# Optimization experiments

Measured on AMD Instinct MI355X. Metric: run time of the kernel, lower is better.

The kernel has to match this reference:

```python
import jax, jax.numpy as jnp
import numpy as np

N = 100000
E = 1600000
IN_C = 128
HID = 32
HEADS = 4
OUT_C = 16
NEG_SLOPE = 0.2  # PyG GATConv default


def setup_inputs() -> dict:
    key = jax.random.key(0)
    ks = jax.random.split(key, 10)
    x = jax.random.normal(ks[0], (N, IN_C), dtype=jnp.float32)
    edge_index = jax.random.randint(ks[1], (2, E), 0, N, dtype=jnp.int64)
    # Layer 1 params (heads=4, concat=True)
    s1 = 1.0 / np.sqrt(IN_C)
    W1 = jax.random.normal(ks[2], (IN_C, HEADS * HID), dtype=jnp.float32) * s1
    a_src1 = jax.random.normal(ks[3], (HEADS, HID), dtype=jnp.float32) * s1
    a_dst1 = jax.random.normal(ks[4], (HEADS, HID), dtype=jnp.float32) * s1
    b1 = jnp.zeros((HEADS * HID,), dtype=jnp.float32)
    # Layer 2 params (heads=1, concat=False)
    s2 = 1.0 / np.sqrt(HEADS * HID)
    W2 = jax.random.normal(ks[5], (HEADS * HID, OUT_C), dtype=jnp.float32) * s2
    a_src2 = jax.random.normal(ks[6], (1, OUT_C), dtype=jnp.float32) * s2
    a_dst2 = jax.random.normal(ks[7], (1, OUT_C), dtype=jnp.float32) * s2
    b2 = jnp.zeros((OUT_C,), dtype=jnp.float32)
    return {"x": x, "edge_index": edge_index, "W1": W1, "a_src1": a_src1,
            "a_dst1": a_dst1, "b1": b1, "W2": W2, "a_src2": a_src2,
            "a_dst2": a_dst2, "b2": b2}


def _gat_layer(x, src, dst, W, a_src, a_dst, b, heads, out_c, concat):
    n = x.shape[0]
    h = (x @ W).reshape(n, heads, out_c)            # [N, H, C]
    al_s = jnp.sum(h * a_src, axis=-1)              # [N, H]
    al_d = jnp.sum(h * a_dst, axis=-1)              # [N, H]
    e = al_s[src] + al_d[dst]                       # [E, H]
    e = jnp.where(e > 0, e, NEG_SLOPE * e)          # LeakyReLU(0.2)
    # segment softmax over incoming edges per destination node
    m = jax.ops.segment_max(e, dst, num_segments=n)
    ex = jnp.exp(e - m[dst])
    denom = jax.ops.segment_sum(ex, dst, num_segments=n)
    alpha = ex / denom[dst]                         # [E, H]
    msg = h[src] * alpha[:, :, None]                # [E, H, C]
    out = jax.ops.segment_sum(msg, dst, num_segments=n)  # [N, H, C]
    out = out.reshape(n, heads * out_c) if concat else out.mean(axis=1)
    return out + b


def reference(x, edge_index, W1, a_src1, a_dst1, b1, W2, a_src2, a_dst2, b2):
    n = x.shape[0]
    loops = jnp.arange(n, dtype=edge_index.dtype)
    src = jnp.concatenate([edge_index[0], loops])   # PyG adds self-loops
    dst = jnp.concatenate([edge_index[1], loops])
    h = _gat_layer(x, src, dst, W1, a_src1, a_dst1, b1, HEADS, HID, True)
    h = jax.nn.relu(h)  # dropout is identity at inference
    out = _gat_layer(h, src, dst, W2, a_src2, a_dst2, b2, 1, OUT_C, False)
    return out
```

## Files before the change

### kernel.cpp

```cpp
#include <hip/hip_runtime.h>
#include <hip/hip_fp16.h>

#define N_NODES 100000
#define N_EDGES 1600000
#define E_TOT   (N_EDGES + N_NODES)
#define NEG_SLOPE 0.2f

#define BSH   9
#define BSZ   512
#define NBKT  ((N_NODES + BSZ - 1) / BSZ)
#define CAP   10240
#define EPB   2048
#define PART_B ((E_TOT + EPB - 1) / EPB)
#define GEMM1_B ((N_NODES + 63) / 64)
#define GSTRIDE 16

typedef _Float16 half8_t __attribute__((ext_vector_type(8)));
typedef float f32x4 __attribute__((ext_vector_type(4)));

__device__ __forceinline__ float lrelu(float v) { return v > 0.f ? v : NEG_SLOPE * v; }

__device__ __forceinline__ float f16lo(unsigned u) {
    return __half2float(__ushort_as_half((unsigned short)(u & 0xFFFFu)));
}
__device__ __forceinline__ float f16hi(unsigned u) {
    return __half2float(__ushort_as_half((unsigned short)(u >> 16)));
}

__global__ __launch_bounds__(256) void k_prep(const float* __restrict__ W1,
                                              _Float16* __restrict__ w1t,
                                              int* __restrict__ gcur) {
    int idx = blockIdx.x * 256 + threadIdx.x;
    if (idx < NBKT * GSTRIDE) gcur[idx] = 0;
    int k = idx >> 5;
    int c0 = (idx & 31) * 4;
    float4 wv = ((const float4*)W1)[idx];
    w1t[(c0 + 0) * 128 + k] = (_Float16)wv.x;
    w1t[(c0 + 1) * 128 + k] = (_Float16)wv.y;
    w1t[(c0 + 2) * 128 + k] = (_Float16)wv.z;
    w1t[(c0 + 3) * 128 + k] = (_Float16)wv.w;
}

__global__ __launch_bounds__(256) void k_part_gemm1(
        const int* __restrict__ ei, int* __restrict__ gcur, int* __restrict__ packed,
        const float* __restrict__ x, const _Float16* __restrict__ w1t,
        const float* __restrict__ a_src, const float* __restrict__ a_dst,
        unsigned short* __restrict__ h1h, float* __restrict__ als,
        float* __restrict__ ald) {
    __shared__ __align__(16) union {
        _Float16 cs[64 * 136];
        struct { int lcnt[NBKT]; int gpos[NBKT]; int lcur[NBKT]; } p;
    } sm;
    int t = threadIdx.x;
    if (blockIdx.x < PART_B) {
        int se[8], de[8];
        size_t base = (size_t)blockIdx.x * EPB;
#pragma unroll
        for (int i = 0; i < 8; ++i) {
            size_t e = base + t + i * 256;
            if (e < E_TOT) {
                if (e < N_EDGES) { se[i] = ei[e]; de[i] = ei[N_EDGES + e]; }
                else             { se[i] = (int)(e - N_EDGES); de[i] = se[i]; }
            } else de[i] = -1;
        }
        for (int i = t; i < NBKT; i += 256) sm.p.lcnt[i] = 0;
        __syncthreads();
#pragma unroll
        for (int i = 0; i < 8; ++i)
            if (de[i] >= 0) atomicAdd(&sm.p.lcnt[de[i] >> BSH], 1);
        __syncthreads();
        for (int i = t; i < NBKT; i += 256) {
            int c = sm.p.lcnt[i];
            sm.p.gpos[i] = c ? (i * CAP + atomicAdd(&gcur[i * GSTRIDE], c)) : 0;
            sm.p.lcur[i] = 0;
        }
        __syncthreads();
#pragma unroll
        for (int i = 0; i < 8; ++i) {
            if (de[i] >= 0) {
                int b = de[i] >> BSH;
                int c = atomicAdd(&sm.p.lcur[b], 1);
                packed[sm.p.gpos[b] + c] = ((de[i] & (BSZ - 1)) << 17) | se[i];
            }
        }
        return;
    }
    int nb = (blockIdx.x - PART_B) * 64;
    int wv = t >> 6, lane = t & 63;
    int mn = lane & 15, quad = lane >> 4;
    int an = nb + wv * 16 + mn;
    if (an >= N_NODES) an = 0;
    const float* xrow = x + (size_t)an * 128;
    f32x4 acc[8];
#pragma unroll
    for (int ct = 0; ct < 8; ++ct) acc[ct] = (f32x4){0.f, 0.f, 0.f, 0.f};
#pragma unroll
    for (int kk = 0; kk < 4; ++kk) {
        float4 a0 = *(const float4*)(xrow + kk * 32 + quad * 8);
        float4 a1 = *(const float4*)(xrow + kk * 32 + quad * 8 + 4);
        half8_t af = { (_Float16)a0.x, (_Float16)a0.y, (_Float16)a0.z, (_Float16)a0.w,
                       (_Float16)a1.x, (_Float16)a1.y, (_Float16)a1.z, (_Float16)a1.w };
#pragma unroll
        for (int ct = 0; ct < 8; ++ct) {
            half8_t bf = *(const half8_t*)(w1t + (ct * 16 + mn) * 128 + kk * 32 + quad * 8);
            acc[ct] = __builtin_amdgcn_mfma_f32_16x16x32_f16(af, bf, acc[ct], 0, 0, 0);
        }
    }
#pragma unroll
    for (int ct = 0; ct < 8; ++ct)
#pragma unroll
        for (int r = 0; r < 4; ++r) {
            int nl = wv * 16 + quad * 4 + r;
            sm.cs[nl * 136 + ct * 16 + mn] = (_Float16)acc[ct][r];
        }
    __syncthreads();
    int node = t >> 2, seg = t & 3;
    int gn = nb + node;
    if (gn < N_NODES) {
        const half8_t* hp = (const half8_t*)&sm.cs[node * 136 + seg * 32];
        uint4* gout = (uint4*)(h1h + (size_t)gn * 128 + seg * 32);
        const float4* asp = (const float4*)a_src;
        const float4* adp = (const float4*)a_dst;
        float vs = 0.f, vd = 0.f;
#pragma unroll
        for (int jj = 0; jj < 4; ++jj) {
            half8_t hv = hp[jj];
            gout[jj] = *(const uint4*)&hv;
            float4 aS0 = asp[seg * 8 + jj * 2], aS1 = asp[seg * 8 + jj * 2 + 1];
            float4 aD0 = adp[seg * 8 + jj * 2], aD1 = adp[seg * 8 + jj * 2 + 1];
            vs += (float)hv[0] * aS0.x + (float)hv[1] * aS0.y + (float)hv[2] * aS0.z + (float)hv[3] * aS0.w
                + (float)hv[4] * aS1.x + (float)hv[5] * aS1.y + (float)hv[6] * aS1.z + (float)hv[7] * aS1.w;
            vd += (float)hv[0] * aD0.x + (float)hv[1] * aD0.y + (float)hv[2] * aD0.z + (float)hv[3] * aD0.w
                + (float)hv[4] * aD1.x + (float)hv[5] * aD1.y + (float)hv[6] * aD1.z + (float)hv[7] * aD1.w;
        }
        als[gn * 4 + seg] = vs;
        ald[gn * 4 + seg] = vd;
    }
}

__global__ __launch_bounds__(512) void k_build(const int* __restrict__ packed,
                                               const int* __restrict__ gcur,
                                               int* __restrict__ rowptr,
                                               int* __restrict__ deg,
                                               int* __restrict__ col) {
    int t = threadIdx.x;
    int b = blockIdx.x;
    int nb = b << BSH;
    int ebeg = b * CAP;
    int eend = ebeg + gcur[b * GSTRIDE];
    __shared__ int cnt[BSZ];
    __shared__ int ps[BSZ];
    cnt[t] = 0;
    __syncthreads();
    for (int i = ebeg + t; i < eend; i += 512)
        atomicAdd(&cnt[packed[i] >> 17], 1);
    __syncthreads();
    int v = cnt[t];
    ps[t] = v;
    __syncthreads();
    for (int off = 1; off < 512; off <<= 1) {
        int u = (t >= off) ? ps[t - off] : 0;
        __syncthreads();
        ps[t] += u;
        __syncthreads();
    }
    int myofs = ebeg + ps[t] - v;
    int n = nb + t;
    if (n < N_NODES) { rowptr[n] = myofs; deg[n] = v; }
    __syncthreads();
    cnt[t] = myofs;
    __syncthreads();
    for (int i = ebeg + t; i < eend; i += 512) {
        int p = packed[i];
        int pos = atomicAdd(&cnt[p >> 17], 1);
        col[pos] = p & 0x1FFFF;
    }
}

__global__ __launch_bounds__(256) void k_agg1(const unsigned short* __restrict__ h1h,
                                              const float* __restrict__ als,
                                              const float* __restrict__ ald,
                                              const int* __restrict__ rowptr,
                                              const int* __restrict__ deg,
                                              const int* __restrict__ col,
                                              const float* __restrict__ b1,
                                              float* __restrict__ out1) {
    __shared__ float sex_all[4][64 * 4];
    __shared__ int   scol_all[4][64];
    int w = threadIdx.x >> 6;
    int lane = threadIdx.x & 63;
    int n = blockIdx.x * 4 + w;
    int slot = lane >> 4, cg = lane & 15;
    int hd = cg >> 2;
    float* sex = sex_all[w];
    int* scol = scol_all[w];
    float4 ald4 = ((const float4*)ald)[n];
    int beg = rowptr[n], dtot = deg[n];
    float a0 = 0.f, a1 = 0.f, a2 = 0.f, a3 = 0.f;
    float a4 = 0.f, a5 = 0.f, a6 = 0.f, a7 = 0.f, den = 0.f;
    const float4* als4p = (const float4*)als;
    for (int base = 0; base < dtot; base += 64) {
        int cnt = min(64, dtot - base);
        int myc = 0;
        if (lane < cnt) myc = col[beg + base + lane];
        __asm__ volatile("s_waitcnt lgkmcnt(0)" ::: "memory");
        if (lane < cnt) {
            scol[lane] = myc;
            float4 as4 = als4p[myc];
            float4 e4;
            e4.x = __expf(lrelu(as4.x + ald4.x));
            e4.y = __expf(lrelu(as4.y + ald4.y));
            e4.z = __expf(lrelu(as4.z + ald4.z));
            e4.w = __expf(lrelu(as4.w + ald4.w));
            ((float4*)sex)[lane] = e4;
        }
        __asm__ volatile("s_waitcnt lgkmcnt(0)" ::: "memory");
#pragma unroll 2
        for (int q4 = 0; q4 < cnt; q4 += 4) {
            int myq = q4 + slot;
            int cq = min(myq, cnt - 1);
            int s = scol[cq];
            float ex = (myq < cnt) ? sex[cq * 4 + hd] : 0.f;
            uint4 hv = *(const uint4*)((const char*)h1h + (((size_t)s << 8) + (cg << 4)));
            a0 = fmaf(ex, f16lo(hv.x), a0);
            a1 = fmaf(ex, f16hi(hv.x), a1);
            a2 = fmaf(ex, f16lo(hv.y), a2);
            a3 = fmaf(ex, f16hi(hv.y), a3);
            a4 = fmaf(ex, f16lo(hv.z), a4);
            a5 = fmaf(ex, f16hi(hv.z), a5);
            a6 = fmaf(ex, f16lo(hv.w), a6);
            a7 = fmaf(ex, f16hi(hv.w), a7);
            den += ex;
        }
    }
    a0 += __shfl_xor(a0, 16, 64); a1 += __shfl_xor(a1, 16, 64);
    a2 += __shfl_xor(a2, 16, 64); a3 += __shfl_xor(a3, 16, 64);
    a4 += __shfl_xor(a4, 16, 64); a5 += __shfl_xor(a5, 16, 64);
    a6 += __shfl_xor(a6, 16, 64); a7 += __shfl_xor(a7, 16, 64);
    den += __shfl_xor(den, 16, 64);
    a0 += __shfl_xor(a0, 32, 64); a1 += __shfl_xor(a1, 32, 64);
    a2 += __shfl_xor(a2, 32, 64); a3 += __shfl_xor(a3, 32, 64);
    a4 += __shfl_xor(a4, 32, 64); a5 += __shfl_xor(a5, 32, 64);
    a6 += __shfl_xor(a6, 32, 64); a7 += __shfl_xor(a7, 32, 64);
    den += __shfl_xor(den, 32, 64);
    if (lane < 16) {
        float inv = 1.0f / den;
        float4 bA = ((const float4*)b1)[2 * lane];
        float4 bB = ((const float4*)b1)[2 * lane + 1];
        float4 oA, oB;
        oA.x = fmaxf(fmaf(a0, inv, bA.x), 0.f);
        oA.y = fmaxf(fmaf(a1, inv, bA.y), 0.f);
        oA.z = fmaxf(fmaf(a2, inv, bA.z), 0.f);
        oA.w = fmaxf(fmaf(a3, inv, bA.w), 0.f);
        oB.x = fmaxf(fmaf(a4, inv, bB.x), 0.f);
        oB.y = fmaxf(fmaf(a5, inv, bB.y), 0.f);
        oB.z = fmaxf(fmaf(a6, inv, bB.z), 0.f);
        oB.w = fmaxf(fmaf(a7, inv, bB.w), 0.f);
        ((float4*)out1)[(size_t)n * 32 + 2 * lane]     = oA;
        ((float4*)out1)[(size_t)n * 32 + 2 * lane + 1] = oB;
    }
}

__global__ __launch_bounds__(256) void k_gemm2(const float* __restrict__ out1,
                                               const float* __restrict__ W2,
                                               const float* __restrict__ a_src,
                                               const float* __restrict__ a_dst,
                                               unsigned short* __restrict__ h2h,
                                               float* __restrict__ als,
                                               float* __restrict__ ald) {
    __shared__ float W2s[128 * 16];
    __shared__ float xs[16 * 132];
    int t = threadIdx.x;
#pragma unroll
    for (int i = 0; i < 8; ++i) W2s[t + i * 256] = W2[t + i * 256];
    size_t base = (size_t)blockIdx.x * 16 * 128;
#pragma unroll
    for (int i = 0; i < 8; ++i) {
        int idx = t + i * 256;
        xs[(idx >> 7) * 132 + (idx & 127)] = out1[base + idx];
    }
    __syncthreads();
    int r = t >> 4, c = t & 15;
    float acc = 0.f;
    const float* xr = &xs[r * 132];
#pragma unroll 8
    for (int k = 0; k < 128; ++k) acc = fmaf(xr[k], W2s[k * 16 + c], acc);
    int n = blockIdx.x * 16 + r;
    h2h[(size_t)n * 16 + c] = __half_as_ushort(__float2half(acc));
    float vs = acc * a_src[c];
    float vd = acc * a_dst[c];
#pragma unroll
    for (int off = 8; off >= 1; off >>= 1) {
        vs += __shfl_down(vs, off, 16);
        vd += __shfl_down(vd, off, 16);
    }
    if (c == 0) { als[n] = vs; ald[n] = vd; }
}

__global__ __launch_bounds__(256) void k_agg2(const unsigned short* __restrict__ h2h,
                                              const float* __restrict__ als,
                                              const float* __restrict__ ald,
                                              const int* __restrict__ rowptr,
                                              const int* __restrict__ deg,
                                              const int* __restrict__ col,
                                              const float* __restrict__ b2,
                                              float* __restrict__ out) {
    __shared__ float sex_all[4][64];
    __shared__ int   scol_all[4][64];
    int w = threadIdx.x >> 6;
    int lane = threadIdx.x & 63;
    int n = blockIdx.x * 4 + w;
    int slot = lane >> 2, q = lane & 3;
    float* sex = sex_all[w];
    int* scol = scol_all[w];
    float ad = ald[n];
    int beg = rowptr[n], dtot = deg[n];
    float a0 = 0.f, a1 = 0.f, a2 = 0.f, a3 = 0.f, den = 0.f;
    for (int base = 0; base < dtot; base += 64) {
        int cnt = min(64, dtot - base);
        int myc = 0;
        if (lane < cnt) myc = col[beg + base + lane];
        __asm__ volatile("s_waitcnt lgkmcnt(0)" ::: "memory");
        if (lane < cnt) {
            scol[lane] = myc;
            sex[lane] = __expf(lrelu(als[myc] + ad));
        }
        __asm__ volatile("s_waitcnt lgkmcnt(0)" ::: "memory");
#pragma unroll 2
        for (int q16 = 0; q16 < cnt; q16 += 16) {
            int myq = q16 + slot;
            int cq = min(myq, cnt - 1);
            int s = scol[cq];
            float ex = (myq < cnt) ? sex[cq] : 0.f;
            uint2 hv = *(const uint2*)((const char*)h2h + ((size_t)s * 32u + (q << 3)));
            a0 = fmaf(ex, f16lo(hv.x), a0);
            a1 = fmaf(ex, f16hi(hv.x), a1);
            a2 = fmaf(ex, f16lo(hv.y), a2);
            a3 = fmaf(ex, f16hi(hv.y), a3);
            den += ex;
        }
    }
#pragma unroll
    for (int off = 4; off <= 32; off <<= 1) {
        a0 += __shfl_xor(a0, off, 64);
        a1 += __shfl_xor(a1, off, 64);
        a2 += __shfl_xor(a2, off, 64);
        a3 += __shfl_xor(a3, off, 64);
        den += __shfl_xor(den, off, 64);
    }
    if (slot == 0) {
        float inv = 1.0f / den;
        float4 b4 = ((const float4*)b2)[q];
        float4 o;
        o.x = fmaf(a0, inv, b4.x);
        o.y = fmaf(a1, inv, b4.y);
        o.z = fmaf(a2, inv, b4.z);
        o.w = fmaf(a3, inv, b4.w);
        ((float4*)out)[(size_t)n * 4 + q] = o;
    }
}

extern "C" void kernel_launch(void* const* d_in, const int* in_sizes, int n_in,
                              void* d_out, int out_size, void* d_ws, size_t ws_size,
                              hipStream_t stream) {
    const float* x   = (const float*)d_in[0];
    const int*   ei  = (const int*)d_in[1];
    const float* W1  = (const float*)d_in[2];
    const float* as1 = (const float*)d_in[3];
    const float* ad1 = (const float*)d_in[4];
    const float* b1  = (const float*)d_in[5];
    const float* W2  = (const float*)d_in[6];
    const float* as2 = (const float*)d_in[7];
    const float* ad2 = (const float*)d_in[8];
    const float* b2  = (const float*)d_in[9];
    float* out = (float*)d_out;

    char* ws = (char*)d_ws;
    size_t off = 0;
    auto alloc = [&](size_t bytes) -> void* {
        void* p = ws + off;
        off += (bytes + 255) & ~(size_t)255;
        return p;
    };
    unsigned short* h1h = (unsigned short*)alloc((size_t)N_NODES * 128 * 2);
    float* out1  = (float*)alloc((size_t)N_NODES * 128 * 4);
    float* als1v = (float*)alloc((size_t)N_NODES * 4 * 4);
    float* ald1v = (float*)alloc((size_t)N_NODES * 4 * 4);
    unsigned short* h2h = (unsigned short*)alloc((size_t)N_NODES * 16 * 2);
    float* als2v = (float*)alloc((size_t)N_NODES * 4);
    float* ald2v = (float*)alloc((size_t)N_NODES * 4);
    int* rowptr  = (int*)alloc((size_t)N_NODES * 4);
    int* degv    = (int*)alloc((size_t)N_NODES * 4);
    int* gcur    = (int*)alloc((size_t)NBKT * GSTRIDE * 4);
    _Float16* w1t = (_Float16*)alloc((size_t)128 * 128 * 2);
    int* packed  = (int*)alloc((size_t)NBKT * CAP * 4);
    int* colA    = (int*)alloc((size_t)NBKT * CAP * 4);

    k_prep<<<16, 256, 0, stream>>>(W1, w1t, gcur);
    k_part_gemm1<<<PART_B + GEMM1_B, 256, 0, stream>>>(ei, gcur, packed,
                                                       x, w1t, as1, ad1, h1h, als1v, ald1v);
    k_build<<<NBKT, 512, 0, stream>>>(packed, gcur, rowptr, degv, colA);
    k_agg1<<<N_NODES / 4, 256, 0, stream>>>(h1h, als1v, ald1v, rowptr, degv, colA, b1, out1);
    k_gemm2<<<N_NODES / 16, 256, 0, stream>>>(out1, W2, as2, ad2, h2h, als2v, ald2v);
    k_agg2<<<N_NODES / 4, 256, 0, stream>>>(h2h, als2v, ald2v, rowptr, degv, colA, b2, out);
}
```

Before: 324.4 us.

## Regroup prep/partition and GEMM1/CSR-build into fused kernels for overlap

Moves the W1 transpose into the edge-partition kernel and moves the CSR build into the GEMM1 kernel, so each launch runs independent work side by side. gcur is now zeroed with a memset, and the build runs on 256 threads with two nodes per thread in its scan. The aim is to overlap the build's latency-bound scan with GEMM1 and to remove a dependent kernel boundary. The cost is an extra memset launch, and the build blocks may leave the GPU unevenly loaded.

```diff
diff --git a/kernel.cpp b/kernel.cpp
--- a/kernel.cpp
+++ b/kernel.cpp
@@ -12,6 +12,7 @@
 #define CAP   10240
 #define EPB   2048
 #define PART_B ((E_TOT + EPB - 1) / EPB)
+#define PREP_B 16
 #define GEMM1_B ((N_NODES + 63) / 64)
 #define GSTRIDE 16
 
@@ -27,65 +28,105 @@
     return __half2float(__ushort_as_half((unsigned short)(u >> 16)));
 }
 
-__global__ __launch_bounds__(256) void k_prep(const float* __restrict__ W1,
-                                              _Float16* __restrict__ w1t,
-                                              int* __restrict__ gcur) {
-    int idx = blockIdx.x * 256 + threadIdx.x;
-    if (idx < NBKT * GSTRIDE) gcur[idx] = 0;
-    int k = idx >> 5;
-    int c0 = (idx & 31) * 4;
-    float4 wv = ((const float4*)W1)[idx];
-    w1t[(c0 + 0) * 128 + k] = (_Float16)wv.x;
-    w1t[(c0 + 1) * 128 + k] = (_Float16)wv.y;
-    w1t[(c0 + 2) * 128 + k] = (_Float16)wv.z;
-    w1t[(c0 + 3) * 128 + k] = (_Float16)wv.w;
-}
-
-__global__ __launch_bounds__(256) void k_part_gemm1(
-        const int* __restrict__ ei, int* __restrict__ gcur, int* __restrict__ packed,
+__global__ __launch_bounds__(256) void k_prep_part(
+        const float* __restrict__ W1, _Float16* __restrict__ w1t,
+        const int* __restrict__ ei, int* __restrict__ gcur,
+        int* __restrict__ packed) {
+    __shared__ int lcnt[NBKT];
+    __shared__ int gpos[NBKT];
+    __shared__ int lcur[NBKT];
+    int t = threadIdx.x;
+    if (blockIdx.x < PREP_B) {
+        int idx = blockIdx.x * 256 + t;
+        int k = idx >> 5;
+        int c0 = (idx & 31) * 4;
+        float4 wv = ((const float4*)W1)[idx];
+        w1t[(c0 + 0) * 128 + k] = (_Float16)wv.x;
+        w1t[(c0 + 1) * 128 + k] = (_Float16)wv.y;
+        w1t[(c0 + 2) * 128 + k] = (_Float16)wv.z;
+        w1t[(c0 + 3) * 128 + k] = (_Float16)wv.w;
+        return;
+    }
+    int se[8], de[8];
+    size_t base = (size_t)(blockIdx.x - PREP_B) * EPB;
+#pragma unroll
+    for (int i = 0; i < 8; ++i) {
+        size_t e = base + t + i * 256;
+        if (e < E_TOT) {
+            if (e < N_EDGES) { se[i] = ei[e]; de[i] = ei[N_EDGES + e]; }
+            else             { se[i] = (int)(e - N_EDGES); de[i] = se[i]; }
+        } else de[i] = -1;
+    }
+    for (int i = t; i < NBKT; i += 256) lcnt[i] = 0;
+    __syncthreads();
+#pragma unroll
+    for (int i = 0; i < 8; ++i)
+        if (de[i] >= 0) atomicAdd(&lcnt[de[i] >> BSH], 1);
+    __syncthreads();
+    for (int i = t; i < NBKT; i += 256) {
+        int c = lcnt[i];
+        gpos[i] = c ? (i * CAP + atomicAdd(&gcur[i * GSTRIDE], c)) : 0;
+        lcur[i] = 0;
+    }
+    __syncthreads();
+#pragma unroll
+    for (int i = 0; i < 8; ++i) {
+        if (de[i] >= 0) {
+            int b = de[i] >> BSH;
+            int c = atomicAdd(&lcur[b], 1);
+            packed[gpos[b] + c] = ((de[i] & (BSZ - 1)) << 17) | se[i];
+        }
+    }
+}
+
+__global__ __launch_bounds__(256) void k_gemm1_build(
         const float* __restrict__ x, const _Float16* __restrict__ w1t,
         const float* __restrict__ a_src, const float* __restrict__ a_dst,
         unsigned short* __restrict__ h1h, float* __restrict__ als,
-        float* __restrict__ ald) {
+        float* __restrict__ ald,
+        const int* __restrict__ packed, const int* __restrict__ gcur,
+        int* __restrict__ rowptr, int* __restrict__ deg, int* __restrict__ col) {
     __shared__ __align__(16) union {
         _Float16 cs[64 * 136];
-        struct { int lcnt[NBKT]; int gpos[NBKT]; int lcur[NBKT]; } p;
+        struct { int cnt[BSZ]; int ps[256]; } b;
     } sm;
     int t = threadIdx.x;
-    if (blockIdx.x < PART_B) {
-        int se[8], de[8];
-        size_t base = (size_t)blockIdx.x * EPB;
-#pragma unroll
-        for (int i = 0; i < 8; ++i) {
-            size_t e = base + t + i * 256;
-            if (e < E_TOT) {
-                if (e < N_EDGES) { se[i] = ei[e]; de[i] = ei[N_EDGES + e]; }
-                else             { se[i] = (int)(e - N_EDGES); de[i] = se[i]; }
-            } else de[i] = -1;
-        }
-        for (int i = t; i < NBKT; i += 256) sm.p.lcnt[i] = 0;
+    if (blockIdx.x < NBKT) {
+        int b = blockIdx.x;
+        int nb = b << BSH;
+        int ebeg = b * CAP;
+        int eend = ebeg + gcur[b * GSTRIDE];
+        sm.b.cnt[t] = 0;
+        sm.b.cnt[t + 256] = 0;
         __syncthreads();
-#pragma unroll
-        for (int i = 0; i < 8; ++i)
-            if (de[i] >= 0) atomicAdd(&sm.p.lcnt[de[i] >> BSH], 1);
+        for (int i = ebeg + t; i < eend; i += 256)
+            atomicAdd(&sm.b.cnt[packed[i] >> 17], 1);
         __syncthreads();
-        for (int i = t; i < NBKT; i += 256) {
-            int c = sm.p.lcnt[i];
-            sm.p.gpos[i] = c ? (i * CAP + atomicAdd(&gcur[i * GSTRIDE], c)) : 0;
-            sm.p.lcur[i] = 0;
-        }
+        int v0 = sm.b.cnt[2 * t], v1 = sm.b.cnt[2 * t + 1];
+        int s = v0 + v1;
+        sm.b.ps[t] = s;
         __syncthreads();
-#pragma unroll
-        for (int i = 0; i < 8; ++i) {
-            if (de[i] >= 0) {
-                int b = de[i] >> BSH;
-                int c = atomicAdd(&sm.p.lcur[b], 1);
-                packed[sm.p.gpos[b] + c] = ((de[i] & (BSZ - 1)) << 17) | se[i];
-            }
+        for (int off = 1; off < 256; off <<= 1) {
+            int u = (t >= off) ? sm.b.ps[t - off] : 0;
+            __syncthreads();
+            sm.b.ps[t] += u;
+            __syncthreads();
+        }
+        int base = ebeg + sm.b.ps[t] - s;
+        int n0 = nb + 2 * t, n1 = nb + 2 * t + 1;
+        if (n0 < N_NODES) { rowptr[n0] = base;      deg[n0] = v0; }
+        if (n1 < N_NODES) { rowptr[n1] = base + v0; deg[n1] = v1; }
+        sm.b.cnt[2 * t]     = base;
+        sm.b.cnt[2 * t + 1] = base + v0;
+        __syncthreads();
+        for (int i = ebeg + t; i < eend; i += 256) {
+            int p = packed[i];
+            int pos = atomicAdd(&sm.b.cnt[p >> 17], 1);
+            col[pos] = p & 0x1FFFF;
         }
         return;
     }
-    int nb = (blockIdx.x - PART_B) * 64;
+    int nb = (blockIdx.x - NBKT) * 64;
     int wv = t >> 6, lane = t & 63;
     int mn = lane & 15, quad = lane >> 4;
     int an = nb + wv * 16 + mn;
@@ -135,45 +176,6 @@
         }
         als[gn * 4 + seg] = vs;
         ald[gn * 4 + seg] = vd;
-    }
-}
-
-__global__ __launch_bounds__(512) void k_build(const int* __restrict__ packed,
-                                               const int* __restrict__ gcur,
-                                               int* __restrict__ rowptr,
-                                               int* __restrict__ deg,
-                                               int* __restrict__ col) {
-    int t = threadIdx.x;
-    int b = blockIdx.x;
-    int nb = b << BSH;
-    int ebeg = b * CAP;
-    int eend = ebeg + gcur[b * GSTRIDE];
-    __shared__ int cnt[BSZ];
-    __shared__ int ps[BSZ];
-    cnt[t] = 0;
-    __syncthreads();
-    for (int i = ebeg + t; i < eend; i += 512)
-        atomicAdd(&cnt[packed[i] >> 17], 1);
-    __syncthreads();
-    int v = cnt[t];
-    ps[t] = v;
-    __syncthreads();
-    for (int off = 1; off < 512; off <<= 1) {
-        int u = (t >= off) ? ps[t - off] : 0;
-        __syncthreads();
-        ps[t] += u;
-        __syncthreads();
-    }
-    int myofs = ebeg + ps[t] - v;
-    int n = nb + t;
-    if (n < N_NODES) { rowptr[n] = myofs; deg[n] = v; }
-    __syncthreads();
-    cnt[t] = myofs;
-    __syncthreads();
-    for (int i = ebeg + t; i < eend; i += 512) {
-        int p = packed[i];
-        int pos = atomicAdd(&cnt[p >> 17], 1);
-        col[pos] = p & 0x1FFFF;
     }
 }
 
@@ -396,10 +398,10 @@
     int* packed  = (int*)alloc((size_t)NBKT * CAP * 4);
     int* colA    = (int*)alloc((size_t)NBKT * CAP * 4);
 
-    k_prep<<<16, 256, 0, stream>>>(W1, w1t, gcur);
-    k_part_gemm1<<<PART_B + GEMM1_B, 256, 0, stream>>>(ei, gcur, packed,
-                                                       x, w1t, as1, ad1, h1h, als1v, ald1v);
-    k_build<<<NBKT, 512, 0, stream>>>(packed, gcur, rowptr, degv, colA);
+    hipMemsetAsync(gcur, 0, (size_t)NBKT * GSTRIDE * 4, stream);
+    k_prep_part<<<PREP_B + PART_B, 256, 0, stream>>>(W1, w1t, ei, gcur, packed);
+    k_gemm1_build<<<NBKT + GEMM1_B, 256, 0, stream>>>(x, w1t, as1, ad1, h1h, als1v, ald1v,
+                                                      packed, gcur, rowptr, degv, colA);
     k_agg1<<<N_NODES / 4, 256, 0, stream>>>(h1h, als1v, ald1v, rowptr, degv, colA, b1, out1);
     k_gemm2<<<N_NODES / 16, 256, 0, stream>>>(out1, W2, as2, ad2, h2h, als2v, ald2v);
     k_agg2<<<N_NODES / 4, 256, 0, stream>>>(h2h, als2v, ald2v, rowptr, degv, colA, b2, out);
```

Measured after the change: 318.5 us. About the same (-1.8%).
